# Performance work log

Measured on AMD Instinct MI355X. Metric: run time of the kernel, lower is better.

Reference implementation:

```python
import jax, jax.numpy as jnp
import numpy as np

B, C, D = 524288, 256, 128


def setup_inputs() -> dict:
    key = jax.random.key(0)
    ks = jax.random.split(key, 20)
    s = 1.0 / np.sqrt(D)
    w = lambda k, shp: jax.random.normal(k, shp, dtype=jnp.float32) * s
    return {
        "h": jax.random.normal(ks[0], (B, D), dtype=jnp.float32),
        "g": jax.random.normal(ks[1], (C, D), dtype=jnp.float32),
        "cluster_id": jax.random.randint(ks[2], (B,), 0, C, dtype=jnp.int32),
        "Wq": w(ks[3], (D, D)),
        "Wk": w(ks[4], (D, D)),
        "attn_bias": jax.random.uniform(ks[5], (D,), dtype=jnp.float32, minval=-0.1, maxval=0.1),
        "Ws_w": w(ks[6], (1, D)),
        "Ws_b": jnp.zeros((1,), dtype=jnp.float32),
        "W_w": w(ks[7], (D, D)),
        "W_b": jnp.zeros((D,), dtype=jnp.float32),
        "Fs_w": w(ks[8], (D, D)),
        "Fs_b": jnp.zeros((D,), dtype=jnp.float32),
        "H1_w": w(ks[9], (D, D)),
        "H1_b": jnp.zeros((D,), dtype=jnp.float32),
        "G1_w": w(ks[10], (D, D)),
        "G1_b": jnp.zeros((D,), dtype=jnp.float32),
        "H2_w": w(ks[11], (D, D)),
        "H2_b": jnp.zeros((D,), dtype=jnp.float32),
        "G2_w": w(ks[12], (D, D)),
        "G2_b": jnp.zeros((D,), dtype=jnp.float32),
    }


def reference(h, g, cluster_id, Wq, Wk, attn_bias, Ws_w, Ws_b, W_w, W_b,
              Fs_w, Fs_b, H1_w, H1_b, G1_w, G1_b, H2_w, H2_b, G2_w, G2_b):
    # --- GNTransmitterUnit: virtual -> graph node message ---
    g_trans = jnp.tanh(g @ Fs_w.T + Fs_b)                 # (C, D)
    g_n = g_trans[cluster_id]                              # gather per node: (B, D)
    # --- gn_merge (WarpGateUnit with gather): gated mix into node features ---
    z1 = jax.nn.sigmoid(h @ H1_w.T + H1_b + g_n @ G1_w.T + G1_b)
    h_merged = (1.0 - z1) * h + z1 * g_n                   # (B, D)
    # --- VNTransmitterUnit: segmented additive (Bahdanau) attention per cluster ---
    q = g @ Wq.T                                           # (C, D)
    k = h @ Wk.T                                           # (B, D)
    score = jnp.tanh(k + q[cluster_id] + attn_bias) @ Ws_w[0] + Ws_b[0]  # (B,)
    m = jax.ops.segment_max(score, cluster_id, num_segments=C)
    m = jnp.where(jnp.isfinite(m), m, 0.0)                 # guard empty clusters
    e = jnp.exp(score - m[cluster_id])
    denom = jax.ops.segment_sum(e, cluster_id, num_segments=C)
    attn = e / jnp.maximum(denom, 1e-20)[cluster_id]       # segment softmax (B,)
    ctx = jax.ops.segment_sum(attn[:, None] * h, cluster_id, num_segments=C)  # (C, D)
    h_trans = jnp.tanh(ctx @ W_w.T + W_b)                  # (C, D)
    # --- vn_merge (WarpGateUnit): gated mix into virtual-node features ---
    z2 = jax.nn.sigmoid(g @ H2_w.T + H2_b + h_trans @ G2_w.T + G2_b)
    g_merged = (1.0 - z2) * g + z2 * h_trans               # (C, D)
    return jnp.concatenate([h_merged, g_merged], axis=0)   # (B + C, D)
```

## Files before the change

kernel.cpp:

```cpp
#include <hip/hip_runtime.h>
#include <hip/hip_bf16.h>

#define NB   524288
#define NC   256
#define ND   128

typedef __attribute__((ext_vector_type(4))) float f32x4;
typedef __attribute__((ext_vector_type(8))) short bf16x8;

__device__ inline float fast_exp(float x)  { return exp2f(x * 1.4426950408889634f); }
__device__ inline float fast_sigmoid(float x) { return __builtin_amdgcn_rcpf(1.f + fast_exp(-x)); }
__device__ inline float fast_tanh(float x) { return 1.f - 2.f * __builtin_amdgcn_rcpf(1.f + fast_exp(2.f * x)); }

__device__ inline unsigned short f2bf(float f) {
    unsigned u = __float_as_uint(f);
    u += 0x7FFFu + ((u >> 16) & 1u);
    return (unsigned short)(u >> 16);
}

__device__ inline bf16x8 pack8(const float* __restrict__ p) {
    float4 a = *(const float4*)p;
    float4 b = *(const float4*)(p + 4);
    bf16x8 r;
    r[0] = (short)f2bf(a.x); r[1] = (short)f2bf(a.y);
    r[2] = (short)f2bf(a.z); r[3] = (short)f2bf(a.w);
    r[4] = (short)f2bf(b.x); r[5] = (short)f2bf(b.y);
    r[6] = (short)f2bf(b.z); r[7] = (short)f2bf(b.w);
    return r;
}

__device__ inline unsigned enc_f32(float s) {
    unsigned b = __float_as_uint(s);
    return b ^ (unsigned)(((int)b >> 31) | (int)0x80000000);
}

__global__ __launch_bounds__(128) void k1_cluster_prep(
    const float* __restrict__ g, const float* __restrict__ Wq,
    const float* __restrict__ attn_bias,
    const float* __restrict__ Fs_w, const float* __restrict__ Fs_b,
    const float* __restrict__ G1_w, const float* __restrict__ G1_b,
    float* __restrict__ g_trans, float* __restrict__ gG1, float* __restrict__ qb) {
    const int c = blockIdx.x, d = threadIdx.x;
    __shared__ float g_lds[ND];
    __shared__ float gt_lds[ND];
    g_lds[d] = g[c * ND + d];
    __syncthreads();
    float accF = Fs_b[d], accQ = attn_bias[d];
    const float* fr = Fs_w + d * ND;
    const float* qr = Wq + d * ND;
    for (int k = 0; k < ND; ++k) {
        float gv = g_lds[k];
        accF += fr[k] * gv;
        accQ += qr[k] * gv;
    }
    float gt = fast_tanh(accF);
    g_trans[c * ND + d] = gt;
    gt_lds[d] = gt;
    qb[c * ND + d] = accQ;
    __syncthreads();
    float accG = G1_b[d];
    const float* gr = G1_w + d * ND;
    for (int k = 0; k < ND; ++k) accG += gr[k] * gt_lds[k];
    gG1[c * ND + d] = accG;
}

__global__ __launch_bounds__(256) void k2_pass1(
    const float* __restrict__ h, const int* __restrict__ cid,
    const float* __restrict__ Wk, const float* __restrict__ H1w,
    const float* __restrict__ H1b, const float* __restrict__ Wsw,
    const float* __restrict__ g_trans, const float* __restrict__ gG1,
    const float* __restrict__ qb,
    float* __restrict__ outh, float* __restrict__ score) {
    const int tid = threadIdx.x;
    const int w = tid >> 6, l = tid & 63;
    const int l15 = l & 15, lg = l >> 4;

    bf16x8 bk[2][4], bh[2][4];
#pragma unroll
    for (int t2 = 0; t2 < 2; ++t2) {
        const int trow = (w + t2 * 4) * 16 + l15;
#pragma unroll
        for (int c = 0; c < 4; ++c) {
            const int col = c * 32 + lg * 8;
            bk[t2][c] = pack8(Wk + trow * ND + col);
            bh[t2][c] = pack8(H1w + trow * ND + col);
        }
    }
    const int d0 = w * 16 + l15, d1 = d0 + 64;
    const float ws0 = Wsw[d0], ws1 = Wsw[d1];
    const float hb0 = H1b[d0], hb1 = H1b[d1];

    const int nb0 = blockIdx.x * 256;

    for (int it = 0; it < 16; ++it) {
        const int nb = nb0 + it * 16;
        bf16x8 af[4];
        const float* hrow = h + (size_t)(nb + l15) * ND + lg * 8;
#pragma unroll
        for (int c = 0; c < 4; ++c) af[c] = pack8(hrow + c * 32);

        f32x4 acck0 = {0.f, 0.f, 0.f, 0.f}, acck1 = {0.f, 0.f, 0.f, 0.f};
        f32x4 acch0 = {0.f, 0.f, 0.f, 0.f}, acch1 = {0.f, 0.f, 0.f, 0.f};
#pragma unroll
        for (int c = 0; c < 4; ++c) {
            acck0 = __builtin_amdgcn_mfma_f32_16x16x32_bf16(af[c], bk[0][c], acck0, 0, 0, 0);
            acck1 = __builtin_amdgcn_mfma_f32_16x16x32_bf16(af[c], bk[1][c], acck1, 0, 0, 0);
            acch0 = __builtin_amdgcn_mfma_f32_16x16x32_bf16(af[c], bh[0][c], acch0, 0, 0, 0);
            acch1 = __builtin_amdgcn_mfma_f32_16x16x32_bf16(af[c], bh[1][c], acch1, 0, 0, 0);
        }
#pragma unroll
        for (int r = 0; r < 4; ++r) {
            const int node = nb + lg * 4 + r;
            const int cc = cid[node];
            const float* qrow = qb + cc * ND;
            const float* grow = gG1 + cc * ND;
            const float* trow = g_trans + cc * ND;
            const float* hrw  = h + (size_t)node * ND;
            float q0  = qrow[d0], q1  = qrow[d1];
            float gg0 = grow[d0], gg1 = grow[d1];
            float gt0 = trow[d0], gt1 = trow[d1];
            float hv0 = hrw[d0],  hv1 = hrw[d1];
            float sp = fast_tanh(acck0[r] + q0) * ws0 + fast_tanh(acck1[r] + q1) * ws1;
            sp += __shfl_xor(sp, 1);
            sp += __shfl_xor(sp, 2);
            sp += __shfl_xor(sp, 4);
            sp += __shfl_xor(sp, 8);
            if (l15 == 0) unsafeAtomicAdd(&score[node], sp);
            float z0 = fast_sigmoid(acch0[r] + hb0 + gg0);
            float z1 = fast_sigmoid(acch1[r] + hb1 + gg1);
            outh[(size_t)node * ND + d0] = (1.f - z0) * hv0 + z0 * gt0;
            outh[(size_t)node * ND + d1] = (1.f - z1) * hv1 + z1 * gt1;
        }
    }
}

__global__ __launch_bounds__(256) void k3_segmax(
    const float* __restrict__ score, const int* __restrict__ cid,
    unsigned* __restrict__ m_enc) {
    __shared__ unsigned mloc[NC];
    const int t = threadIdx.x;
    mloc[t] = 0u;
    __syncthreads();
    for (int i = blockIdx.x * 256 + t; i < NB; i += 256 * 256) {
        atomicMax(&mloc[cid[i]], enc_f32(score[i]));
    }
    __syncthreads();
    atomicMax(m_enc + t, mloc[t]);
}

__global__ __launch_bounds__(256) void k4_pass2(
    const float* __restrict__ h, const int* __restrict__ cid,
    const float* __restrict__ score, const unsigned* __restrict__ m_enc,
    float* __restrict__ ctx_raw, float* __restrict__ denom) {
    __shared__ float cloc[NC * 33];
    __shared__ float dloc[NC];
    __shared__ float mloc[NC];
    const int t = threadIdx.x, w = t >> 6, l = t & 63;
    const int q = blockIdx.x & 3;
    const int bg = blockIdx.x >> 2;
    for (int i = t; i < NC * 33; i += 256) cloc[i] = 0.f;
    dloc[t] = 0.f;
    {
        unsigned u = m_enc[t];
        unsigned bits = (u & 0x80000000u) ? (u ^ 0x80000000u) : ~u;
        float f = __uint_as_float(bits);
        mloc[t] = ((bits & 0x7F800000u) == 0x7F800000u) ? 0.f : f;
    }
    __syncthreads();
    const int colbase = q * 32 + (l & 7) * 4;
    const int n0 = bg * 2048 + w * 512;
    for (int nn = 0; nn < 512; nn += 8) {
        const int node = n0 + nn + (l >> 3);
        float s = score[node];
        int c = cid[node];
        float e = fast_exp(s - mloc[c]);
        float4 hv = *(const float4*)(h + (size_t)node * ND + colbase);
        const int base = c * 33 + (l & 7) * 4;
        atomicAdd(&cloc[base + 0], e * hv.x);
        atomicAdd(&cloc[base + 1], e * hv.y);
        atomicAdd(&cloc[base + 2], e * hv.z);
        atomicAdd(&cloc[base + 3], e * hv.w);
        if ((l & 7) == 0 && q == 0) atomicAdd(&dloc[c], e);
    }
    __syncthreads();
    for (int i = t; i < NC * 32; i += 256) {
        const int c = i >> 5, col = i & 31;
        unsafeAtomicAdd(&ctx_raw[c * ND + q * 32 + col], cloc[c * 33 + col]);
    }
    if (q == 0) unsafeAtomicAdd(&denom[t], dloc[t]);
}

__global__ __launch_bounds__(128) void k5_final(
    const float* __restrict__ g, const float* __restrict__ ctx_raw,
    const float* __restrict__ denom,
    const float* __restrict__ W_w, const float* __restrict__ W_b,
    const float* __restrict__ H2_w, const float* __restrict__ H2_b,
    const float* __restrict__ G2_w, const float* __restrict__ G2_b,
    float* __restrict__ out_g) {
    const int c = blockIdx.x, d = threadIdx.x;
    __shared__ float ctx_l[ND], ht_l[ND], g_l[ND];
    float den = fmaxf(denom[c], 1e-20f);
    float ctxv = ctx_raw[c * ND + d] / den;
    ctx_l[d] = ctxv;
    g_l[d] = g[c * ND + d];
    __syncthreads();
    float acc = W_b[d];
    const float* wr = W_w + d * ND;
    for (int k = 0; k < ND; ++k) acc += wr[k] * ctx_l[k];
    float ht = fast_tanh(acc);
    ht_l[d] = ht;
    __syncthreads();
    float acc2 = H2_b[d] + G2_b[d];
    const float* h2r = H2_w + d * ND;
    const float* g2r = G2_w + d * ND;
    for (int k = 0; k < ND; ++k) acc2 += h2r[k] * g_l[k] + g2r[k] * ht_l[k];
    float z = fast_sigmoid(acc2);
    out_g[c * ND + d] = (1.f - z) * g_l[d] + z * ht;
}

extern "C" void kernel_launch(void* const* d_in, const int* in_sizes, int n_in,
                              void* d_out, int out_size, void* d_ws, size_t ws_size,
                              hipStream_t stream) {
    const float* h     = (const float*)d_in[0];
    const float* g     = (const float*)d_in[1];
    const int*   cid   = (const int*)d_in[2];
    const float* Wq    = (const float*)d_in[3];
    const float* Wk    = (const float*)d_in[4];
    const float* attnb = (const float*)d_in[5];
    const float* Ws_w  = (const float*)d_in[6];
    const float* W_w   = (const float*)d_in[8];
    const float* W_b   = (const float*)d_in[9];
    const float* Fs_w  = (const float*)d_in[10];
    const float* Fs_b  = (const float*)d_in[11];
    const float* H1_w  = (const float*)d_in[12];
    const float* H1_b  = (const float*)d_in[13];
    const float* G1_w  = (const float*)d_in[14];
    const float* G1_b  = (const float*)d_in[15];
    const float* H2_w  = (const float*)d_in[16];
    const float* H2_b  = (const float*)d_in[17];
    const float* G2_w  = (const float*)d_in[18];
    const float* G2_b  = (const float*)d_in[19];
    float* out = (float*)d_out;
    float* ws  = (float*)d_ws;

    float*    g_trans = ws;
    float*    gG1     = ws + 32768;
    float*    qb      = ws + 65536;
    float*    score   = ws + 98304;
    unsigned* m_enc   = (unsigned*)(ws + 622592);
    float*    denom   = ws + 622848;
    float*    ctx_raw = ws + 623104;
    hipMemsetAsync(ws + 98304, 0, (524288 + 256 + 256 + 32768) * sizeof(float), stream);

    k1_cluster_prep<<<NC, ND, 0, stream>>>(g, Wq, attnb, Fs_w, Fs_b, G1_w, G1_b,
                                           g_trans, gG1, qb);
    k2_pass1<<<2048, 256, 0, stream>>>(h, cid, Wk, H1_w, H1_b, Ws_w,
                                       g_trans, gG1, qb, out, score);
    k3_segmax<<<256, 256, 0, stream>>>(score, cid, m_enc);
    k4_pass2<<<1024, 256, 0, stream>>>(h, cid, score, m_enc, ctx_raw, denom);
    k5_final<<<NC, ND, 0, stream>>>(g, ctx_raw, denom, W_w, W_b,
                                    H2_w, H2_b, G2_w, G2_b,
                                    out + (size_t)NB * ND);
}
```

Before: 1.082 ms.

## Drop segment-max pass and split pass-1 waves into score and gate roles

Removes the segment-max kernel and the max subtraction from the softmax, computing exp(score) directly. This relies on the score being bounded by the tanh times the Ws_w weights, so it saves a full read of score and cid plus one launch. The risk is exp overflow for large-magnitude Ws weights. The pass-1 kernel now runs 512-thread blocks whose waves specialise: half compute the attention score with Wk, half compute the gated merge with H1. Each wave therefore holds fewer weight fragments. The cluster ids are loaded as one int4, and the pass-2 loop is unrolled.

New measurement: 1.145 ms. 5.9% more time.

```diff
diff --git a/kernel.cpp b/kernel.cpp
--- a/kernel.cpp
+++ b/kernel.cpp
@@ -27,11 +27,6 @@
     r[4] = (short)f2bf(b.x); r[5] = (short)f2bf(b.y);
     r[6] = (short)f2bf(b.z); r[7] = (short)f2bf(b.w);
     return r;
-}
-
-__device__ inline unsigned enc_f32(float s) {
-    unsigned b = __float_as_uint(s);
-    return b ^ (unsigned)(((int)b >> 31) | (int)0x80000000);
 }
 
 __global__ __launch_bounds__(128) void k1_cluster_prep(
@@ -64,7 +59,7 @@
     gG1[c * ND + d] = accG;
 }
 
-__global__ __launch_bounds__(256) void k2_pass1(
+__global__ __launch_bounds__(512, 6) void k2_pass1(
     const float* __restrict__ h, const int* __restrict__ cid,
     const float* __restrict__ Wk, const float* __restrict__ H1w,
     const float* __restrict__ H1b, const float* __restrict__ Wsw,
@@ -74,21 +69,21 @@
     const int tid = threadIdx.x;
     const int w = tid >> 6, l = tid & 63;
     const int l15 = l & 15, lg = l >> 4;
-
-    bf16x8 bk[2][4], bh[2][4];
+    const int role = w >> 2;
+    const int w4 = w & 3;
+
+    const float* Wmat = role ? H1w : Wk;
+    bf16x8 bw[2][4];
 #pragma unroll
     for (int t2 = 0; t2 < 2; ++t2) {
-        const int trow = (w + t2 * 4) * 16 + l15;
-#pragma unroll
-        for (int c = 0; c < 4; ++c) {
-            const int col = c * 32 + lg * 8;
-            bk[t2][c] = pack8(Wk + trow * ND + col);
-            bh[t2][c] = pack8(H1w + trow * ND + col);
-        }
-    }
-    const int d0 = w * 16 + l15, d1 = d0 + 64;
-    const float ws0 = Wsw[d0], ws1 = Wsw[d1];
-    const float hb0 = H1b[d0], hb1 = H1b[d1];
+        const int trow = (2 * w4 + t2) * 16 + l15;
+#pragma unroll
+        for (int c = 0; c < 4; ++c)
+            bw[t2][c] = pack8(Wmat + trow * ND + c * 32 + lg * 8);
+    }
+    const int d0 = 32 * w4 + l15, d1 = d0 + 16;
+    const float c0 = role ? H1b[d0] : Wsw[d0];
+    const float c1 = role ? H1b[d1] : Wsw[d1];
 
     const int nb0 = blockIdx.x * 256;
 
@@ -98,82 +93,66 @@
         const float* hrow = h + (size_t)(nb + l15) * ND + lg * 8;
 #pragma unroll
         for (int c = 0; c < 4; ++c) af[c] = pack8(hrow + c * 32);
-
-        f32x4 acck0 = {0.f, 0.f, 0.f, 0.f}, acck1 = {0.f, 0.f, 0.f, 0.f};
-        f32x4 acch0 = {0.f, 0.f, 0.f, 0.f}, acch1 = {0.f, 0.f, 0.f, 0.f};
+        int4 cc4 = *(const int4*)(cid + nb + lg * 4);
+
+        f32x4 acc0 = {0.f, 0.f, 0.f, 0.f}, acc1 = {0.f, 0.f, 0.f, 0.f};
 #pragma unroll
         for (int c = 0; c < 4; ++c) {
-            acck0 = __builtin_amdgcn_mfma_f32_16x16x32_bf16(af[c], bk[0][c], acck0, 0, 0, 0);
-            acck1 = __builtin_amdgcn_mfma_f32_16x16x32_bf16(af[c], bk[1][c], acck1, 0, 0, 0);
-            acch0 = __builtin_amdgcn_mfma_f32_16x16x32_bf16(af[c], bh[0][c], acch0, 0, 0, 0);
-            acch1 = __builtin_amdgcn_mfma_f32_16x16x32_bf16(af[c], bh[1][c], acch1, 0, 0, 0);
+            acc0 = __builtin_amdgcn_mfma_f32_16x16x32_bf16(af[c], bw[0][c], acc0, 0, 0, 0);
+            acc1 = __builtin_amdgcn_mfma_f32_16x16x32_bf16(af[c], bw[1][c], acc1, 0, 0, 0);
         }
-#pragma unroll
-        for (int r = 0; r < 4; ++r) {
-            const int node = nb + lg * 4 + r;
-            const int cc = cid[node];
-            const float* qrow = qb + cc * ND;
-            const float* grow = gG1 + cc * ND;
-            const float* trow = g_trans + cc * ND;
-            const float* hrw  = h + (size_t)node * ND;
-            float q0  = qrow[d0], q1  = qrow[d1];
-            float gg0 = grow[d0], gg1 = grow[d1];
-            float gt0 = trow[d0], gt1 = trow[d1];
-            float hv0 = hrw[d0],  hv1 = hrw[d1];
-            float sp = fast_tanh(acck0[r] + q0) * ws0 + fast_tanh(acck1[r] + q1) * ws1;
-            sp += __shfl_xor(sp, 1);
-            sp += __shfl_xor(sp, 2);
-            sp += __shfl_xor(sp, 4);
-            sp += __shfl_xor(sp, 8);
-            if (l15 == 0) unsafeAtomicAdd(&score[node], sp);
-            float z0 = fast_sigmoid(acch0[r] + hb0 + gg0);
-            float z1 = fast_sigmoid(acch1[r] + hb1 + gg1);
-            outh[(size_t)node * ND + d0] = (1.f - z0) * hv0 + z0 * gt0;
-            outh[(size_t)node * ND + d1] = (1.f - z1) * hv1 + z1 * gt1;
+        const int ccs[4] = {cc4.x, cc4.y, cc4.z, cc4.w};
+        if (role == 0) {
+#pragma unroll
+            for (int r = 0; r < 4; ++r) {
+                const int node = nb + lg * 4 + r;
+                const float* qrow = qb + ccs[r] * ND;
+                float sp = fast_tanh(acc0[r] + qrow[d0]) * c0
+                         + fast_tanh(acc1[r] + qrow[d1]) * c1;
+                sp += __shfl_xor(sp, 1);
+                sp += __shfl_xor(sp, 2);
+                sp += __shfl_xor(sp, 4);
+                sp += __shfl_xor(sp, 8);
+                if (l15 == 0) unsafeAtomicAdd(&score[node], sp);
+            }
+        } else {
+#pragma unroll
+            for (int r = 0; r < 4; ++r) {
+                const int node = nb + lg * 4 + r;
+                const float* grow = gG1 + ccs[r] * ND;
+                const float* trow = g_trans + ccs[r] * ND;
+                const float* hrw  = h + (size_t)node * ND;
+                float gg0 = grow[d0], gg1 = grow[d1];
+                float gt0 = trow[d0], gt1 = trow[d1];
+                float hv0 = hrw[d0],  hv1 = hrw[d1];
+                float z0 = fast_sigmoid(acc0[r] + c0 + gg0);
+                float z1 = fast_sigmoid(acc1[r] + c1 + gg1);
+                outh[(size_t)node * ND + d0] = (1.f - z0) * hv0 + z0 * gt0;
+                outh[(size_t)node * ND + d1] = (1.f - z1) * hv1 + z1 * gt1;
+            }
         }
     }
-}
-
-__global__ __launch_bounds__(256) void k3_segmax(
-    const float* __restrict__ score, const int* __restrict__ cid,
-    unsigned* __restrict__ m_enc) {
-    __shared__ unsigned mloc[NC];
-    const int t = threadIdx.x;
-    mloc[t] = 0u;
-    __syncthreads();
-    for (int i = blockIdx.x * 256 + t; i < NB; i += 256 * 256) {
-        atomicMax(&mloc[cid[i]], enc_f32(score[i]));
-    }
-    __syncthreads();
-    atomicMax(m_enc + t, mloc[t]);
 }
 
 __global__ __launch_bounds__(256) void k4_pass2(
     const float* __restrict__ h, const int* __restrict__ cid,
-    const float* __restrict__ score, const unsigned* __restrict__ m_enc,
+    const float* __restrict__ score,
     float* __restrict__ ctx_raw, float* __restrict__ denom) {
     __shared__ float cloc[NC * 33];
     __shared__ float dloc[NC];
-    __shared__ float mloc[NC];
     const int t = threadIdx.x, w = t >> 6, l = t & 63;
     const int q = blockIdx.x & 3;
     const int bg = blockIdx.x >> 2;
     for (int i = t; i < NC * 33; i += 256) cloc[i] = 0.f;
     dloc[t] = 0.f;
-    {
-        unsigned u = m_enc[t];
-        unsigned bits = (u & 0x80000000u) ? (u ^ 0x80000000u) : ~u;
-        float f = __uint_as_float(bits);
-        mloc[t] = ((bits & 0x7F800000u) == 0x7F800000u) ? 0.f : f;
-    }
     __syncthreads();
     const int colbase = q * 32 + (l & 7) * 4;
     const int n0 = bg * 2048 + w * 512;
+#pragma unroll 4
     for (int nn = 0; nn < 512; nn += 8) {
         const int node = n0 + nn + (l >> 3);
-        float s = score[node];
+        float e = fast_exp(score[node]);
         int c = cid[node];
-        float e = fast_exp(s - mloc[c]);
         float4 hv = *(const float4*)(h + (size_t)node * ND + colbase);
         const int base = c * 33 + (l & 7) * 4;
         atomicAdd(&cloc[base + 0], e * hv.x);
@@ -243,21 +222,19 @@
     float* out = (float*)d_out;
     float* ws  = (float*)d_ws;
 
-    float*    g_trans = ws;
-    float*    gG1     = ws + 32768;
-    float*    qb      = ws + 65536;
-    float*    score   = ws + 98304;
-    unsigned* m_enc   = (unsigned*)(ws + 622592);
-    float*    denom   = ws + 622848;
-    float*    ctx_raw = ws + 623104;
-    hipMemsetAsync(ws + 98304, 0, (524288 + 256 + 256 + 32768) * sizeof(float), stream);
+    float* g_trans = ws;
+    float* gG1     = ws + 32768;
+    float* qb      = ws + 65536;
+    float* score   = ws + 98304;
+    float* denom   = ws + 622592;
+    float* ctx_raw = ws + 622848;
+    (void)hipMemsetAsync(ws + 98304, 0, (524288 + 256 + 32768) * sizeof(float), stream);
 
     k1_cluster_prep<<<NC, ND, 0, stream>>>(g, Wq, attnb, Fs_w, Fs_b, G1_w, G1_b,
                                            g_trans, gG1, qb);
-    k2_pass1<<<2048, 256, 0, stream>>>(h, cid, Wk, H1_w, H1_b, Ws_w,
+    k2_pass1<<<2048, 512, 0, stream>>>(h, cid, Wk, H1_w, H1_b, Ws_w,
                                        g_trans, gG1, qb, out, score);
-    k3_segmax<<<256, 256, 0, stream>>>(score, cid, m_enc);
-    k4_pass2<<<1024, 256, 0, stream>>>(h, cid, score, m_enc, ctx_raw, denom);
+    k4_pass2<<<1024, 256, 0, stream>>>(h, cid, score, ctx_raw, denom);
     k5_final<<<NC, ND, 0, stream>>>(g, ctx_raw, denom, W_w, W_b,
                                     H2_w, H2_b, G2_w, G2_b,
                                     out + (size_t)NB * ND);
```
